# Kernel optimization log

Measured on AMD Instinct MI355X. Metric: run time of the kernel, lower is better.

## Reference

```python
import jax, jax.numpy as jnp
import numpy as np

K = 3    # kernel_size
PAD = 1  # floor(K/2) * padding_flag


def ste_sign(x):
    # Binarize to {-1, 0, +1} (torch.sign semantics) with straight-through
    # gradient (identity), matching BNN training where grads flow to weight.org.
    return x + jax.lax.stop_gradient(jnp.sign(x) - x)


def setup_inputs() -> dict:
    key = jax.random.key(0)
    k1, k2 = jax.random.split(key)
    B, Ci, H, W = 16, 64, 32, 32
    Co = 64
    x = jax.random.normal(k1, (B, Ci, H, W), dtype=jnp.float32)
    # weight layout per module: (c_out, k, k, c_in)
    weight = jax.random.normal(k2, (Co, K, K, Ci), dtype=jnp.float32)
    return {"x": x, "weight": weight}


def reference(x, weight):
    # Majority convolution (MajorityNet): binarize input and weight to +/-1,
    # form XNOR-style products over each KxK window, take the MAJORITY (sign of
    # the spatial popcount) PER input channel, then sum majorities over input
    # channels. This is NOT a plain sum-of-products conv.
    B, Ci, H, W = x.shape
    Co = weight.shape[0]

    xb = ste_sign(x)                      # [B,Ci,H,W]  (input.size(1)!=3 -> binarized)
    wb = ste_sign(weight)                 # [Co,K,K,Ci]

    xp = jnp.pad(xb, ((0, 0), (0, 0), (PAD, PAD), (PAD, PAD)))

    # s[b,co,ci,y,x] = sum_{dy,dx} xb[b,ci,y+dy,x+dx] * wb[co,dy,dx,ci]
    s = jnp.zeros((B, Co, Ci, H, W), x.dtype)
    for dy in range(K):          # fixed K*K=9-iteration loop, fused under jit
        for dx in range(K):
            s = s + xp[:, None, :, dy:dy + H, dx:dx + W] \
                    * wb[None, :, dy, dx, :, None, None]

    # majority per input channel, then accumulate across input channels
    out = ste_sign(s).sum(axis=2)         # [B,Co,H,W]
    return out
```

## Files before the change

kernel.cpp:

```cpp
#include <hip/hip_runtime.h>
#include <stdint.h>

#define BB 16
#define CI 64
#define CO 64
#define HH 32
#define WW 32

__device__ __forceinline__ void fadd(uint32_t a, uint32_t b, uint32_t c,
                                     uint32_t& s, uint32_t& cy) {
    uint32_t t = a ^ b;
    s = t ^ c;
    cy = (t & c) | (a & b);
}
__device__ __forceinline__ void hadd(uint32_t a, uint32_t b, uint32_t& s, uint32_t& cy) {
    s = a ^ b;
    cy = a & b;
}
__device__ __forceinline__ void add5(const uint32_t* a, const uint32_t* b, uint32_t* r) {
    uint32_t c;
    hadd(a[0], b[0], r[0], c);
#pragma unroll
    for (int k = 1; k < 5; ++k) fadd(a[k], b[k], c, r[k], c);
    r[5] = c;
}
__device__ __forceinline__ void add6(const uint32_t* a, const uint32_t* b, uint32_t* r) {
    uint32_t c;
    hadd(a[0], b[0], r[0], c);
#pragma unroll
    for (int k = 1; k < 6; ++k) fadd(a[k], b[k], c, r[k], c);
    r[6] = c;
}

__global__ __launch_bounds__(256) void pack_kernel(const float* __restrict__ x,
                                                   const float* __restrict__ w,
                                                   uint32_t* __restrict__ xbits,
                                                   uint32_t* __restrict__ winv) {
    const int bid = blockIdx.x;
    const int tid = threadIdx.x;
    if (bid < 512) {
        const int base = bid * 2048;
#pragma unroll
        for (int it = 0; it < 8; ++it) {
            int p = base + it * 256 + tid;
            unsigned long long mask = __ballot(x[p] > 0.0f);
            int lane = tid & 63;
            if ((lane & 31) == 0)
                xbits[p >> 5] = (lane & 32) ? (uint32_t)(mask >> 32) : (uint32_t)mask;
        }
    } else {
        int idx = (bid - 512) * 256 + tid;
        int ci = idx & 63, co = idx >> 6;
        uint32_t bits = 0;
#pragma unroll
        for (int t = 0; t < 9; ++t)
            bits |= (w[(co * 9 + t) * CI + ci] > 0.f ? 1u : 0u) << t;
        winv[ci * CO + co] = bits ^ 0x1FFu;
    }
}

__global__ __launch_bounds__(256) void core_kernel(const uint32_t* __restrict__ xbits,
                                                   const uint32_t* __restrict__ winv,
                                                   float* __restrict__ out) {
    __shared__ uint32_t wlds[CI * CO];
    __shared__ uint4 xr4[CI];
    __shared__ uint32_t xnb[2][CI];
    __shared__ uint32_t red[4][CO][5];
    __shared__ uint32_t planes7[CO][7];
    __shared__ int bord[CO][2][2];

    const int bid = blockIdx.x;
    const int tid = threadIdx.x;

    if (bid < BB * HH) {
        const int b = bid >> 5, y = bid & 31;
        if (y == 0 || y == HH - 1) return;

        {
            const uint4* src = (const uint4*)winv;
            uint4* dst = (uint4*)wlds;
#pragma unroll
            for (int i = 0; i < 4; ++i) dst[tid + i * 256] = src[tid + i * 256];
        }
        for (int i = tid; i < 192 + 128; i += 256) {
            if (i < 192) {
                int r = i >> 6, ci = i & 63;
                ((uint32_t*)&xr4[ci])[r] = xbits[(b * CI + ci) * HH + (y - 1 + r)];
            } else {
                int k = i - 192;
                int side = k >> 6, ci = k & 63;
                const uint32_t* rp = &xbits[(b * CI + ci) * HH + (y - 1)];
                uint32_t r0 = rp[0], r1 = rp[1], r2 = rp[2];
                uint32_t n0, n1, n2;
                if (side == 0) {
                    n0 = (r0 & 3u) << 1; n1 = (r1 & 3u) << 1; n2 = (r2 & 3u) << 1;
                } else {
                    n0 = (r0 >> 30) & 3u; n1 = (r1 >> 30) & 3u; n2 = (r2 >> 30) & 3u;
                }
                xnb[side][ci] = n0 | (n1 << 3) | (n2 << 6);
            }
        }
        __syncthreads();

        const int co = tid & 63, ciq = tid >> 6;

        uint32_t maj[16];
#pragma unroll
        for (int i = 0; i < 16; ++i) {
            const int ci = ciq * 16 + i;
            const uint4 xr = xr4[ci];
            const uint32_t wn = wlds[ci * CO + co];
            const uint32_t T0 = xr.x << 1, T1 = xr.x, T2 = xr.x >> 1;
            const uint32_t T3 = xr.y << 1, T4 = xr.y, T5 = xr.y >> 1;
            const uint32_t T6 = xr.z << 1, T7 = xr.z, T8 = xr.z >> 1;
            const uint32_t m0 = T0 ^ (uint32_t)(-(int)((wn >> 0) & 1));
            const uint32_t m1 = T1 ^ (uint32_t)(-(int)((wn >> 1) & 1));
            const uint32_t m2 = T2 ^ (uint32_t)(-(int)((wn >> 2) & 1));
            const uint32_t m3 = T3 ^ (uint32_t)(-(int)((wn >> 3) & 1));
            const uint32_t m4 = T4 ^ (uint32_t)(-(int)((wn >> 4) & 1));
            const uint32_t m5 = T5 ^ (uint32_t)(-(int)((wn >> 5) & 1));
            const uint32_t m6 = T6 ^ (uint32_t)(-(int)((wn >> 6) & 1));
            const uint32_t m7 = T7 ^ (uint32_t)(-(int)((wn >> 7) & 1));
            const uint32_t m8 = T8 ^ (uint32_t)(-(int)((wn >> 8) & 1));
            uint32_t s1, c1, s2, c2, s3, c3, S, C, D, E;
            fadd(m0, m1, m2, s1, c1);
            fadd(m3, m4, m5, s2, c2);
            fadd(m6, m7, m8, s3, c3);
            fadd(s1, s2, s3, S, C);
            fadd(c1, c2, c3, D, E);
            maj[i] = (E & (S | C | D)) | (~E & (S & C & D));
        }

        uint32_t A[5], Bw[5];
        fadd(maj[0], maj[1], maj[2], A[0], Bw[0]);
        fadd(maj[3], maj[4], maj[5], A[1], Bw[1]);
        fadd(maj[6], maj[7], maj[8], A[2], Bw[2]);
        fadd(maj[9], maj[10], maj[11], A[3], Bw[3]);
        fadd(maj[12], maj[13], maj[14], A[4], Bw[4]);
        uint32_t u1, v1, u2, v2, p0, v3;
        fadd(A[0], A[1], A[2], u1, v1);
        fadd(A[3], A[4], maj[15], u2, v2);
        hadd(u1, u2, p0, v3);
        uint32_t e1, f1, e2, f2, e3, f3, p1, f4;
        fadd(Bw[0], Bw[1], Bw[2], e1, f1);
        fadd(Bw[3], Bw[4], v1, e2, f2);
        fadd(e1, e2, v2, e3, f3);
        hadd(e3, v3, p1, f4);
        uint32_t g1, h1, p2, h2, p3, p4;
        fadd(f1, f2, f3, g1, h1);
        hadd(g1, f4, p2, h2);
        hadd(h1, h2, p3, p4);
        red[ciq][co][0] = p0; red[ciq][co][1] = p1; red[ciq][co][2] = p2;
        red[ciq][co][3] = p3; red[ciq][co][4] = p4;

        {
            const int fco = tid & 63, side = (tid >> 6) & 1, cih = tid >> 7;
            const uint32_t vmask = side ? 0x0DBu : 0x1B6u;
            const uint32_t lut = 0xAAA40u;
            int acc = 0;
#pragma unroll 4
            for (int i = 0; i < 32; ++i) {
                const int ci = cih * 32 + i;
                const uint32_t xn = xnb[side][ci];
                const uint32_t wn = wlds[ci * CO + fco];
                const uint32_t mm = (uint32_t)__popc((xn ^ wn) & vmask);
                acc += (lut >> (2 * mm)) & 3u;
            }
            bord[fco][side][cih] = acc;
        }
        __syncthreads();

        if (tid < 64) {
            uint32_t x0[6], x1[6], rr[7];
            add5(red[0][tid], red[1][tid], x0);
            add5(red[2][tid], red[3][tid], x1);
            add6(x0, x1, rr);
#pragma unroll
            for (int k = 0; k < 7; ++k) planes7[tid][k] = rr[k];
        }
        __syncthreads();

        {
            const int oco = tid & 63, q = tid >> 6;
            uint32_t pl[7];
#pragma unroll
            for (int k = 0; k < 7; ++k) pl[k] = planes7[oco][k];
            float vals[8];
#pragma unroll
            for (int j = 0; j < 8; ++j) {
                const int px = q * 8 + j;
                uint32_t cnt = 0;
#pragma unroll
                for (int k = 0; k < 7; ++k) cnt += ((pl[k] >> px) & 1u) << k;
                vals[j] = (float)(2 * (int)cnt - CI);
            }
            if (q == 0) vals[0] = (float)(bord[oco][0][0] + bord[oco][0][1] - CI);
            if (q == 3) vals[7] = (float)(bord[oco][1][0] + bord[oco][1][1] - CI);
            float4* op = (float4*)&out[((size_t)(b * CO + oco) * HH + y) * WW + q * 8];
            op[0] = make_float4(vals[0], vals[1], vals[2], vals[3]);
            op[1] = make_float4(vals[4], vals[5], vals[6], vals[7]);
        }
    } else {
        const int idx = bid - BB * HH;
        const int b = idx >> 3, yb = (idx >> 2) & 1, coq = idx & 3;
        const int y = yb * (HH - 1);
        for (int i = tid; i < CI * 16; i += 256) {
            int ci = i >> 4, c = i & 15;
            wlds[i] = winv[ci * CO + coq * 16 + c];
        }
        if (tid < 3 * CI) {
            int r = tid >> 6, ci = tid & 63;
            int yy = y - 1 + r;
            ((uint32_t*)&xr4[ci])[r] = (yy >= 0 && yy < HH) ? xbits[(b * CI + ci) * HH + yy] : 0u;
        }
        __syncthreads();

        const int px = tid & 31, cog = tid >> 5;
        const uint32_t rowm = (px > 0 ? 1u : 0u) | 2u | (px < WW - 1 ? 4u : 0u);
        const uint32_t vmask = (y > 0 ? rowm : 0u) | (rowm << 3) |
                               (y < HH - 1 ? (rowm << 6) : 0u);
        const uint32_t N = __popc(vmask);
        const uint32_t nt1 = N >> 1, nt2 = (N - 1) >> 1;
        uint32_t lut = 0;
        for (uint32_t m = 1; m <= 9; ++m)
            lut |= (uint32_t)((m > nt1) + (m > nt2)) << (2 * m);
        int a0 = 0, a1 = 0;
        for (int ci = 0; ci < CI; ++ci) {
            const uint4 xr = xr4[ci];
            const uint32_t n0 = (uint32_t)((((uint64_t)xr.x) << 1) >> px) & 7u;
            const uint32_t n1 = (uint32_t)((((uint64_t)xr.y) << 1) >> px) & 7u;
            const uint32_t n2 = (uint32_t)((((uint64_t)xr.z) << 1) >> px) & 7u;
            const uint32_t xn = n0 | (n1 << 3) | (n2 << 6);
            const uint32_t w0 = wlds[ci * 16 + cog * 2 + 0];
            const uint32_t w1 = wlds[ci * 16 + cog * 2 + 1];
            uint32_t mm;
            mm = (uint32_t)__popc((xn ^ w0) & vmask); a0 += (lut >> (2 * mm)) & 3u;
            mm = (uint32_t)__popc((xn ^ w1) & vmask); a1 += (lut >> (2 * mm)) & 3u;
        }
        const int co0 = coq * 16 + cog * 2;
        out[((size_t)(b * CO + co0 + 0) * HH + y) * WW + px] = (float)(a0 - CI);
        out[((size_t)(b * CO + co0 + 1) * HH + y) * WW + px] = (float)(a1 - CI);
    }
}

extern "C" void kernel_launch(void* const* d_in, const int* in_sizes, int n_in,
                              void* d_out, int out_size, void* d_ws, size_t ws_size,
                              hipStream_t stream) {
    const float* x = (const float*)d_in[0];
    const float* w = (const float*)d_in[1];
    float* out = (float*)d_out;

    uint32_t* xbits = (uint32_t*)d_ws;
    uint32_t* winv = xbits + BB * CI * HH;

    pack_kernel<<<512 + 16, 256, 0, stream>>>(x, w, xbits, winv);
    core_kernel<<<BB * HH + 128, 256, 0, stream>>>(xbits, winv, out);
}
```

Measured before the change: 21.35 us.

## Fuse input binarization into core kernel, packing rows from float x

The input sign-packing step moves out of the separate pack kernel and into the core kernel. Each block now reads the three float rows it needs straight from x and packs them with wave ballots into shared memory, so the xbits workspace round trip is gone. The pack kernel now only handles the weights. In exchange, every input row is read and binarized about three times (once per neighbouring output row), which raises global float traffic in the core kernel.

Result: slower. 26.26 us (+23.0%).

```diff
diff --git a/kernel.cpp b/kernel.cpp
--- a/kernel.cpp
+++ b/kernel.cpp
@@ -32,34 +32,18 @@
     r[6] = c;
 }
 
-__global__ __launch_bounds__(256) void pack_kernel(const float* __restrict__ x,
-                                                   const float* __restrict__ w,
-                                                   uint32_t* __restrict__ xbits,
-                                                   uint32_t* __restrict__ winv) {
-    const int bid = blockIdx.x;
-    const int tid = threadIdx.x;
-    if (bid < 512) {
-        const int base = bid * 2048;
-#pragma unroll
-        for (int it = 0; it < 8; ++it) {
-            int p = base + it * 256 + tid;
-            unsigned long long mask = __ballot(x[p] > 0.0f);
-            int lane = tid & 63;
-            if ((lane & 31) == 0)
-                xbits[p >> 5] = (lane & 32) ? (uint32_t)(mask >> 32) : (uint32_t)mask;
-        }
-    } else {
-        int idx = (bid - 512) * 256 + tid;
-        int ci = idx & 63, co = idx >> 6;
-        uint32_t bits = 0;
-#pragma unroll
-        for (int t = 0; t < 9; ++t)
-            bits |= (w[(co * 9 + t) * CI + ci] > 0.f ? 1u : 0u) << t;
-        winv[ci * CO + co] = bits ^ 0x1FFu;
-    }
-}
-
-__global__ __launch_bounds__(256) void core_kernel(const uint32_t* __restrict__ xbits,
+__global__ __launch_bounds__(256) void packw_kernel(const float* __restrict__ w,
+                                                    uint32_t* __restrict__ winv) {
+    int idx = blockIdx.x * 256 + threadIdx.x;
+    int ci = idx & 63, co = idx >> 6;
+    uint32_t bits = 0;
+#pragma unroll
+    for (int t = 0; t < 9; ++t)
+        bits |= (w[(co * 9 + t) * CI + ci] > 0.f ? 1u : 0u) << t;
+    winv[ci * CO + co] = bits ^ 0x1FFu;
+}
+
+__global__ __launch_bounds__(256) void core_kernel(const float* __restrict__ x,
                                                    const uint32_t* __restrict__ winv,
                                                    float* __restrict__ out) {
     __shared__ uint32_t wlds[CI * CO];
@@ -82,23 +66,30 @@
 #pragma unroll
             for (int i = 0; i < 4; ++i) dst[tid + i * 256] = src[tid + i * 256];
         }
-        for (int i = tid; i < 192 + 128; i += 256) {
-            if (i < 192) {
-                int r = i >> 6, ci = i & 63;
-                ((uint32_t*)&xr4[ci])[r] = xbits[(b * CI + ci) * HH + (y - 1 + r)];
+        {
+            const int wave = tid >> 6, lane = tid & 63;
+            const int half = lane >> 5, px = lane & 31;
+#pragma unroll
+            for (int j = 0; j < 24; ++j) {
+                int task = wave * 48 + j * 2 + half;
+                int r = task >> 6, ci = task & 63;
+                float v = x[((b * CI + ci) * HH + (y - 1 + r)) * WW + px];
+                unsigned long long mask = __ballot(v > 0.f);
+                if (px == 0)
+                    ((uint32_t*)&xr4[ci])[r] = (uint32_t)(half ? (mask >> 32) : mask);
+            }
+        }
+        __syncthreads();
+        if (tid < 128) {
+            int side = tid >> 6, ci = tid & 63;
+            uint4 xr = xr4[ci];
+            uint32_t n0, n1, n2;
+            if (side == 0) {
+                n0 = (xr.x & 3u) << 1; n1 = (xr.y & 3u) << 1; n2 = (xr.z & 3u) << 1;
             } else {
-                int k = i - 192;
-                int side = k >> 6, ci = k & 63;
-                const uint32_t* rp = &xbits[(b * CI + ci) * HH + (y - 1)];
-                uint32_t r0 = rp[0], r1 = rp[1], r2 = rp[2];
-                uint32_t n0, n1, n2;
-                if (side == 0) {
-                    n0 = (r0 & 3u) << 1; n1 = (r1 & 3u) << 1; n2 = (r2 & 3u) << 1;
-                } else {
-                    n0 = (r0 >> 30) & 3u; n1 = (r1 >> 30) & 3u; n2 = (r2 >> 30) & 3u;
-                }
-                xnb[side][ci] = n0 | (n1 << 3) | (n2 << 6);
-            }
+                n0 = (xr.x >> 30) & 3u; n1 = (xr.y >> 30) & 3u; n2 = (xr.z >> 30) & 3u;
+            }
+            xnb[side][ci] = n0 | (n1 << 3) | (n2 << 6);
         }
         __syncthreads();
 
@@ -208,10 +199,19 @@
             int ci = i >> 4, c = i & 15;
             wlds[i] = winv[ci * CO + coq * 16 + c];
         }
-        if (tid < 3 * CI) {
-            int r = tid >> 6, ci = tid & 63;
-            int yy = y - 1 + r;
-            ((uint32_t*)&xr4[ci])[r] = (yy >= 0 && yy < HH) ? xbits[(b * CI + ci) * HH + yy] : 0u;
+        {
+            const int wave = tid >> 6, lane = tid & 63;
+            const int half = lane >> 5, px = lane & 31;
+#pragma unroll
+            for (int j = 0; j < 24; ++j) {
+                int task = wave * 48 + j * 2 + half;
+                int r = task >> 6, ci = task & 63;
+                int yy = y - 1 + r;
+                float v = (yy >= 0 && yy < HH) ? x[((b * CI + ci) * HH + yy) * WW + px] : 0.f;
+                unsigned long long mask = __ballot(v > 0.f);
+                if (px == 0)
+                    ((uint32_t*)&xr4[ci])[r] = (uint32_t)(half ? (mask >> 32) : mask);
+            }
         }
         __syncthreads();
 
@@ -250,9 +250,8 @@
     const float* w = (const float*)d_in[1];
     float* out = (float*)d_out;
 
-    uint32_t* xbits = (uint32_t*)d_ws;
-    uint32_t* winv = xbits + BB * CI * HH;
-
-    pack_kernel<<<512 + 16, 256, 0, stream>>>(x, w, xbits, winv);
-    core_kernel<<<BB * HH + 128, 256, 0, stream>>>(xbits, winv, out);
-}
+    uint32_t* winv = (uint32_t*)d_ws;
+
+    packw_kernel<<<16, 256, 0, stream>>>(w, winv);
+    core_kernel<<<BB * HH + 128, 256, 0, stream>>>(x, winv, out);
+}
```

## Compute two output rows per block and split output channels across block pairs

Applied to the files above, without the earlier changes.

Interior blocks now each handle two adjacent output rows for half of the output channels, instead of one row for all channels. Four input rows are loaded so the middle two rows are shared between both outputs, and the weight tile in shared memory is halved. The per-thread carry-save reduction is reorganised into 8-input groups with a wider final adder tree. Block count stays about the same, but per-block instruction count and reduction depth change. The early-return idle blocks at rows 0 and 31 are removed.

Measured after the change: 20.71 us. 3.0% less time.

```diff
diff --git a/kernel.cpp b/kernel.cpp
--- a/kernel.cpp
+++ b/kernel.cpp
@@ -17,19 +17,47 @@
     s = a ^ b;
     cy = a & b;
 }
-__device__ __forceinline__ void add5(const uint32_t* a, const uint32_t* b, uint32_t* r) {
+__device__ __forceinline__ void add4p(const uint32_t* a, const uint32_t* b, uint32_t* r) {
     uint32_t c;
     hadd(a[0], b[0], r[0], c);
 #pragma unroll
+    for (int k = 1; k < 4; ++k) fadd(a[k], b[k], c, r[k], c);
+    r[4] = c;
+}
+__device__ __forceinline__ void add5p(const uint32_t* a, const uint32_t* b, uint32_t* r) {
+    uint32_t c;
+    hadd(a[0], b[0], r[0], c);
+#pragma unroll
     for (int k = 1; k < 5; ++k) fadd(a[k], b[k], c, r[k], c);
     r[5] = c;
 }
-__device__ __forceinline__ void add6(const uint32_t* a, const uint32_t* b, uint32_t* r) {
+__device__ __forceinline__ void add6p(const uint32_t* a, const uint32_t* b, uint32_t* r) {
     uint32_t c;
     hadd(a[0], b[0], r[0], c);
 #pragma unroll
     for (int k = 1; k < 6; ++k) fadd(a[k], b[k], c, r[k], c);
     r[6] = c;
+}
+__device__ __forceinline__ uint32_t maj9(uint32_t m0, uint32_t m1, uint32_t m2,
+                                         uint32_t m3, uint32_t m4, uint32_t m5,
+                                         uint32_t m6, uint32_t m7, uint32_t m8) {
+    uint32_t s1, c1, s2, c2, s3, c3, S, C, D, E;
+    fadd(m0, m1, m2, s1, c1);
+    fadd(m3, m4, m5, s2, c2);
+    fadd(m6, m7, m8, s3, c3);
+    fadd(s1, s2, s3, S, C);
+    fadd(c1, c2, c3, D, E);
+    return (E & (S | C | D)) | (~E & (S & C & D));
+}
+__device__ __forceinline__ void csa8(const uint32_t* m, uint32_t* p) {
+    uint32_t s1, c1, s2, c2, s3, c3, c4, s5, c5, c6;
+    fadd(m[0], m[1], m[2], s1, c1);
+    fadd(m[3], m[4], m[5], s2, c2);
+    hadd(m[6], m[7], s3, c3);
+    fadd(s1, s2, s3, p[0], c4);
+    fadd(c1, c2, c3, s5, c5);
+    hadd(s5, c4, p[1], c6);
+    hadd(c5, c6, p[2], p[3]);
 }
 
 __global__ __launch_bounds__(256) void pack_kernel(const float* __restrict__ x,
@@ -62,129 +90,130 @@
 __global__ __launch_bounds__(256) void core_kernel(const uint32_t* __restrict__ xbits,
                                                    const uint32_t* __restrict__ winv,
                                                    float* __restrict__ out) {
-    __shared__ uint32_t wlds[CI * CO];
+    __shared__ uint32_t wlds[CI * 32];
     __shared__ uint4 xr4[CI];
-    __shared__ uint32_t xnb[2][CI];
-    __shared__ uint32_t red[4][CO][5];
-    __shared__ uint32_t planes7[CO][7];
-    __shared__ int bord[CO][2][2];
+    __shared__ uint32_t xnb[2][2][CI];
+    __shared__ uint32_t red[2][8][32][4];
+    __shared__ uint32_t planes7[2][32][7];
+    __shared__ int bord[2][32][2][4];
 
     const int bid = blockIdx.x;
     const int tid = threadIdx.x;
 
-    if (bid < BB * HH) {
-        const int b = bid >> 5, y = bid & 31;
-        if (y == 0 || y == HH - 1) return;
+    if (bid < 480) {
+        const int b = bid / 30;
+        const int rem = bid - b * 30;
+        const int pi = rem >> 1, ch = rem & 1;
+        const int y0 = 2 * pi + 1;
 
         {
             const uint4* src = (const uint4*)winv;
             uint4* dst = (uint4*)wlds;
 #pragma unroll
-            for (int i = 0; i < 4; ++i) dst[tid + i * 256] = src[tid + i * 256];
-        }
-        for (int i = tid; i < 192 + 128; i += 256) {
-            if (i < 192) {
-                int r = i >> 6, ci = i & 63;
-                ((uint32_t*)&xr4[ci])[r] = xbits[(b * CI + ci) * HH + (y - 1 + r)];
+            for (int u = 0; u < 2; ++u) {
+                int k = tid + u * 256;
+                int ci = k >> 3, q = k & 7;
+                dst[ci * 8 + q] = src[ci * 16 + ch * 8 + q];
+            }
+        }
+        {
+            int r = tid >> 6, ci = tid & 63;
+            ((uint32_t*)&xr4[ci])[r] = xbits[(b * CI + ci) * HH + (y0 - 1 + r)];
+        }
+        __syncthreads();
+
+        {
+            int row = tid >> 7, side = (tid >> 6) & 1, ci = tid & 63;
+            uint4 xr = xr4[ci];
+            uint32_t r0 = row ? xr.y : xr.x;
+            uint32_t r1 = row ? xr.z : xr.y;
+            uint32_t r2 = row ? xr.w : xr.z;
+            uint32_t n0, n1, n2;
+            if (side == 0) {
+                n0 = (r0 & 3u) << 1; n1 = (r1 & 3u) << 1; n2 = (r2 & 3u) << 1;
             } else {
-                int k = i - 192;
-                int side = k >> 6, ci = k & 63;
-                const uint32_t* rp = &xbits[(b * CI + ci) * HH + (y - 1)];
-                uint32_t r0 = rp[0], r1 = rp[1], r2 = rp[2];
-                uint32_t n0, n1, n2;
-                if (side == 0) {
-                    n0 = (r0 & 3u) << 1; n1 = (r1 & 3u) << 1; n2 = (r2 & 3u) << 1;
-                } else {
-                    n0 = (r0 >> 30) & 3u; n1 = (r1 >> 30) & 3u; n2 = (r2 >> 30) & 3u;
-                }
-                xnb[side][ci] = n0 | (n1 << 3) | (n2 << 6);
-            }
-        }
-        __syncthreads();
-
-        const int co = tid & 63, ciq = tid >> 6;
-
-        uint32_t maj[16];
-#pragma unroll
-        for (int i = 0; i < 16; ++i) {
-            const int ci = ciq * 16 + i;
+                n0 = (r0 >> 30) & 3u; n1 = (r1 >> 30) & 3u; n2 = (r2 >> 30) & 3u;
+            }
+            xnb[row][side][ci] = n0 | (n1 << 3) | (n2 << 6);
+        }
+
+        const int co_l = tid & 31, ciq = tid >> 5;
+
+        uint32_t maj0[8], maj1[8];
+#pragma unroll
+        for (int i = 0; i < 8; ++i) {
+            const int ci = ciq * 8 + i;
             const uint4 xr = xr4[ci];
-            const uint32_t wn = wlds[ci * CO + co];
-            const uint32_t T0 = xr.x << 1, T1 = xr.x, T2 = xr.x >> 1;
-            const uint32_t T3 = xr.y << 1, T4 = xr.y, T5 = xr.y >> 1;
-            const uint32_t T6 = xr.z << 1, T7 = xr.z, T8 = xr.z >> 1;
-            const uint32_t m0 = T0 ^ (uint32_t)(-(int)((wn >> 0) & 1));
-            const uint32_t m1 = T1 ^ (uint32_t)(-(int)((wn >> 1) & 1));
-            const uint32_t m2 = T2 ^ (uint32_t)(-(int)((wn >> 2) & 1));
-            const uint32_t m3 = T3 ^ (uint32_t)(-(int)((wn >> 3) & 1));
-            const uint32_t m4 = T4 ^ (uint32_t)(-(int)((wn >> 4) & 1));
-            const uint32_t m5 = T5 ^ (uint32_t)(-(int)((wn >> 5) & 1));
-            const uint32_t m6 = T6 ^ (uint32_t)(-(int)((wn >> 6) & 1));
-            const uint32_t m7 = T7 ^ (uint32_t)(-(int)((wn >> 7) & 1));
-            const uint32_t m8 = T8 ^ (uint32_t)(-(int)((wn >> 8) & 1));
-            uint32_t s1, c1, s2, c2, s3, c3, S, C, D, E;
-            fadd(m0, m1, m2, s1, c1);
-            fadd(m3, m4, m5, s2, c2);
-            fadd(m6, m7, m8, s3, c3);
-            fadd(s1, s2, s3, S, C);
-            fadd(c1, c2, c3, D, E);
-            maj[i] = (E & (S | C | D)) | (~E & (S & C & D));
-        }
-
-        uint32_t A[5], Bw[5];
-        fadd(maj[0], maj[1], maj[2], A[0], Bw[0]);
-        fadd(maj[3], maj[4], maj[5], A[1], Bw[1]);
-        fadd(maj[6], maj[7], maj[8], A[2], Bw[2]);
-        fadd(maj[9], maj[10], maj[11], A[3], Bw[3]);
-        fadd(maj[12], maj[13], maj[14], A[4], Bw[4]);
-        uint32_t u1, v1, u2, v2, p0, v3;
-        fadd(A[0], A[1], A[2], u1, v1);
-        fadd(A[3], A[4], maj[15], u2, v2);
-        hadd(u1, u2, p0, v3);
-        uint32_t e1, f1, e2, f2, e3, f3, p1, f4;
-        fadd(Bw[0], Bw[1], Bw[2], e1, f1);
-        fadd(Bw[3], Bw[4], v1, e2, f2);
-        fadd(e1, e2, v2, e3, f3);
-        hadd(e3, v3, p1, f4);
-        uint32_t g1, h1, p2, h2, p3, p4;
-        fadd(f1, f2, f3, g1, h1);
-        hadd(g1, f4, p2, h2);
-        hadd(h1, h2, p3, p4);
-        red[ciq][co][0] = p0; red[ciq][co][1] = p1; red[ciq][co][2] = p2;
-        red[ciq][co][3] = p3; red[ciq][co][4] = p4;
-
-        {
-            const int fco = tid & 63, side = (tid >> 6) & 1, cih = tid >> 7;
+            const uint32_t wn = wlds[ci * 32 + co_l];
+            uint32_t S0 = (uint32_t)(-(int)((wn >> 0) & 1));
+            uint32_t S1 = (uint32_t)(-(int)((wn >> 1) & 1));
+            uint32_t S2 = (uint32_t)(-(int)((wn >> 2) & 1));
+            uint32_t S3 = (uint32_t)(-(int)((wn >> 3) & 1));
+            uint32_t S4 = (uint32_t)(-(int)((wn >> 4) & 1));
+            uint32_t S5 = (uint32_t)(-(int)((wn >> 5) & 1));
+            uint32_t S6 = (uint32_t)(-(int)((wn >> 6) & 1));
+            uint32_t S7 = (uint32_t)(-(int)((wn >> 7) & 1));
+            uint32_t S8 = (uint32_t)(-(int)((wn >> 8) & 1));
+            const uint32_t l0 = xr.x << 1, h0 = xr.x >> 1;
+            const uint32_t l1 = xr.y << 1, h1 = xr.y >> 1;
+            const uint32_t l2 = xr.z << 1, h2 = xr.z >> 1;
+            const uint32_t l3 = xr.w << 1, h3 = xr.w >> 1;
+            maj0[i] = maj9(l0 ^ S0, xr.x ^ S1, h0 ^ S2,
+                           l1 ^ S3, xr.y ^ S4, h1 ^ S5,
+                           l2 ^ S6, xr.z ^ S7, h2 ^ S8);
+            maj1[i] = maj9(l1 ^ S0, xr.y ^ S1, h1 ^ S2,
+                           l2 ^ S3, xr.z ^ S4, h2 ^ S5,
+                           l3 ^ S6, xr.w ^ S7, h3 ^ S8);
+        }
+        uint32_t p[4];
+        csa8(maj0, p);
+        *(uint4*)&red[0][ciq][co_l][0] = make_uint4(p[0], p[1], p[2], p[3]);
+        csa8(maj1, p);
+        *(uint4*)&red[1][ciq][co_l][0] = make_uint4(p[0], p[1], p[2], p[3]);
+        __syncthreads();
+
+        {
+            const int fco = tid & 31, side = (tid >> 5) & 1, cq = (tid >> 6) & 3;
             const uint32_t vmask = side ? 0x0DBu : 0x1B6u;
             const uint32_t lut = 0xAAA40u;
-            int acc = 0;
+            int a0 = 0, a1 = 0;
 #pragma unroll 4
-            for (int i = 0; i < 32; ++i) {
-                const int ci = cih * 32 + i;
-                const uint32_t xn = xnb[side][ci];
-                const uint32_t wn = wlds[ci * CO + fco];
-                const uint32_t mm = (uint32_t)__popc((xn ^ wn) & vmask);
-                acc += (lut >> (2 * mm)) & 3u;
-            }
-            bord[fco][side][cih] = acc;
-        }
-        __syncthreads();
-
+            for (int i = 0; i < 16; ++i) {
+                const int ci = cq * 16 + i;
+                const uint32_t wn = wlds[ci * 32 + fco];
+                uint32_t mm0 = (uint32_t)__popc((xnb[0][side][ci] ^ wn) & vmask);
+                uint32_t mm1 = (uint32_t)__popc((xnb[1][side][ci] ^ wn) & vmask);
+                a0 += (lut >> (2 * mm0)) & 3u;
+                a1 += (lut >> (2 * mm1)) & 3u;
+            }
+            bord[0][fco][side][cq] = a0;
+            bord[1][fco][side][cq] = a1;
+        }
         if (tid < 64) {
-            uint32_t x0[6], x1[6], rr[7];
-            add5(red[0][tid], red[1][tid], x0);
-            add5(red[2][tid], red[3][tid], x1);
-            add6(x0, x1, rr);
-#pragma unroll
-            for (int k = 0; k < 7; ++k) planes7[tid][k] = rr[k];
-        }
-        __syncthreads();
-
-        {
-            const int oco = tid & 63, q = tid >> 6;
+            const int row = tid >> 5, col = tid & 31;
+            uint32_t g[8][4];
+#pragma unroll
+            for (int k = 0; k < 8; ++k)
+                *(uint4*)&g[k][0] = *(const uint4*)&red[row][k][col][0];
+            uint32_t t01[5], t23[5], t45[5], t67[5], u0[6], u1[6], rr[7];
+            add4p(g[0], g[1], t01);
+            add4p(g[2], g[3], t23);
+            add4p(g[4], g[5], t45);
+            add4p(g[6], g[7], t67);
+            add5p(t01, t23, u0);
+            add5p(t45, t67, u1);
+            add6p(u0, u1, rr);
+#pragma unroll
+            for (int k = 0; k < 7; ++k) planes7[row][col][k] = rr[k];
+        }
+        __syncthreads();
+
+        {
+            const int row = tid >> 7, r2 = tid & 127;
+            const int col = r2 >> 2, q = r2 & 3;
             uint32_t pl[7];
 #pragma unroll
-            for (int k = 0; k < 7; ++k) pl[k] = planes7[oco][k];
+            for (int k = 0; k < 7; ++k) pl[k] = planes7[row][col][k];
             float vals[8];
 #pragma unroll
             for (int j = 0; j < 8; ++j) {
@@ -194,14 +223,19 @@
                 for (int k = 0; k < 7; ++k) cnt += ((pl[k] >> px) & 1u) << k;
                 vals[j] = (float)(2 * (int)cnt - CI);
             }
-            if (q == 0) vals[0] = (float)(bord[oco][0][0] + bord[oco][0][1] - CI);
-            if (q == 3) vals[7] = (float)(bord[oco][1][0] + bord[oco][1][1] - CI);
-            float4* op = (float4*)&out[((size_t)(b * CO + oco) * HH + y) * WW + q * 8];
+            if (q == 0)
+                vals[0] = (float)(bord[row][col][0][0] + bord[row][col][0][1] +
+                                  bord[row][col][0][2] + bord[row][col][0][3] - CI);
+            if (q == 3)
+                vals[7] = (float)(bord[row][col][1][0] + bord[row][col][1][1] +
+                                  bord[row][col][1][2] + bord[row][col][1][3] - CI);
+            const int co = ch * 32 + col, y = y0 + row;
+            float4* op = (float4*)&out[((size_t)(b * CO + co) * HH + y) * WW + q * 8];
             op[0] = make_float4(vals[0], vals[1], vals[2], vals[3]);
             op[1] = make_float4(vals[4], vals[5], vals[6], vals[7]);
         }
     } else {
-        const int idx = bid - BB * HH;
+        const int idx = bid - 480;
         const int b = idx >> 3, yb = (idx >> 2) & 1, coq = idx & 3;
         const int y = yb * (HH - 1);
         for (int i = tid; i < CI * 16; i += 256) {
@@ -254,5 +288,5 @@
     uint32_t* winv = xbits + BB * CI * HH;
 
     pack_kernel<<<512 + 16, 256, 0, stream>>>(x, w, xbits, winv);
-    core_kernel<<<BB * HH + 128, 256, 0, stream>>>(xbits, winv, out);
-}
+    core_kernel<<<480 + 128, 256, 0, stream>>>(xbits, winv, out);
+}
```
